# Kernel optimization log

Hardware: AMD Instinct MI355X
Metric: run time of the kernel (lower is better)

## Reference

```python
import jax, jax.numpy as jnp
import numpy as np

N, E, G = 50000, 1250000, 256
IN, H, OUT = 64, 64, 2


def _glorot(k, shape):
    fan = shape[0] + shape[1]
    return jax.random.normal(k, shape, jnp.float32) * np.float32(np.sqrt(2.0 / fan))


def setup_inputs() -> dict:
    key = jax.random.key(0)
    ks = jax.random.split(key, 24)
    inp = {
        "x": jax.random.normal(ks[0], (N, IN), jnp.float32),
        "edge_index": jax.random.randint(ks[1], (2, E), 0, N, dtype=jnp.int32),
        "edge_weight": jax.random.uniform(ks[2], (E,), jnp.float32),
        "batch": jnp.sort(jax.random.randint(ks[3], (N,), 0, G, dtype=jnp.int32)),
    }
    # TransformerConv layer 1 (in=IN -> out=H, heads=1, edge_dim=1)
    inp["Wq1"] = _glorot(ks[4], (IN, H)); inp["bq1"] = jnp.zeros((H,), jnp.float32)
    inp["Wk1"] = _glorot(ks[5], (IN, H)); inp["bk1"] = jnp.zeros((H,), jnp.float32)
    inp["Wv1"] = _glorot(ks[6], (IN, H)); inp["bv1"] = jnp.zeros((H,), jnp.float32)
    inp["We1"] = _glorot(ks[7], (1, H))
    inp["Ws1"] = _glorot(ks[8], (IN, H)); inp["bs1"] = jnp.zeros((H,), jnp.float32)
    # TransformerConv layer 2 (H -> H)
    inp["Wq2"] = _glorot(ks[9], (H, H)); inp["bq2"] = jnp.zeros((H,), jnp.float32)
    inp["Wk2"] = _glorot(ks[10], (H, H)); inp["bk2"] = jnp.zeros((H,), jnp.float32)
    inp["Wv2"] = _glorot(ks[11], (H, H)); inp["bv2"] = jnp.zeros((H,), jnp.float32)
    inp["We2"] = _glorot(ks[12], (1, H))
    inp["Ws2"] = _glorot(ks[13], (H, H)); inp["bs2"] = jnp.zeros((H,), jnp.float32)
    # final linear
    inp["Wl"] = _glorot(ks[14], (H, OUT)); inp["bl"] = jnp.zeros((OUT,), jnp.float32)
    return inp


def _tconv(x, src, dst, e_attr, Wq, bq, Wk, bk, Wv, bv, We, Ws, bs, n):
    # PyG TransformerConv, heads=1, concat=True, root_weight=True, beta=False.
    d = Wq.shape[1]
    q = (x @ Wq + bq)[dst]            # [E, d] gather at target nodes
    k = (x @ Wk + bk)[src]            # [E, d] gather at source nodes
    v = (x @ Wv + bv)[src]            # [E, d]
    e = e_attr @ We                   # [E, d] edge embedding (no bias in PyG)
    alpha = jnp.sum(q * (k + e), axis=-1) / jnp.sqrt(jnp.float32(d))  # [E]
    # segment softmax over incoming edges of each target node
    amax = jax.ops.segment_max(alpha, dst, num_segments=n)
    amax = jnp.where(jnp.isfinite(amax), amax, jnp.float32(0.0))
    ex = jnp.exp(alpha - amax[dst])
    denom = jax.ops.segment_sum(ex, dst, num_segments=n)
    w = ex / jnp.maximum(denom[dst], jnp.float32(1e-16))
    out = jax.ops.segment_sum(w[:, None] * (v + e), dst, num_segments=n)  # [n, d]
    return out + x @ Ws + bs          # skip connection (lin_skip)


def reference(x, edge_index, edge_weight, batch,
              Wq1, bq1, Wk1, bk1, Wv1, bv1, We1, Ws1, bs1,
              Wq2, bq2, Wk2, bk2, Wv2, bv2, We2, Ws2, bs2,
              Wl, bl):
    src, dst = edge_index[0], edge_index[1]
    ea = edge_weight[:, None]  # edge_weight.unsqueeze(-1), edge_dim=1
    n = x.shape[0]
    h = jax.nn.relu(_tconv(x, src, dst, ea, Wq1, bq1, Wk1, bk1, Wv1, bv1, We1, Ws1, bs1, n))
    h = jax.nn.relu(_tconv(h, src, dst, ea, Wq2, bq2, Wk2, bk2, Wv2, bv2, We2, Ws2, bs2, n))
    # global_mean_pool over batch ids
    cnt = jax.ops.segment_sum(jnp.ones((n,), jnp.float32), batch, num_segments=G)
    pooled = jax.ops.segment_sum(h, batch, num_segments=G) / jnp.maximum(cnt, 1.0)[:, None]
    return pooled @ Wl + bl
```

## Files before the change

kernel.cpp:

```cpp
#include <hip/hip_runtime.h>
#include <hip/hip_fp16.h>

#define NN 50000
#define NE 1250000
#define NE4 312500
#define NG 256
#define NBKT 782
#define BCAP 2048
#define TILE 4096
#define NTB 306
#define NLIN 999
#define FGRID 1332

#define QSCALE 0.18033688011112042f
#define EXP2 __builtin_amdgcn_exp2f

#if defined(__has_builtin)
#  if __has_builtin(__builtin_amdgcn_fdot2)
#    define HAS_FDOT2 1
#  endif
#endif

typedef _Float16 h2vec __attribute__((ext_vector_type(2)));

static __device__ __forceinline__ float fdot2f(unsigned a, unsigned b, float c) {
#ifdef HAS_FDOT2
    return __builtin_amdgcn_fdot2(__builtin_bit_cast(h2vec, a),
                                  __builtin_bit_cast(h2vec, b), c, false);
#else
    float2 fa = __half22float2(__builtin_bit_cast(__half2, a));
    float2 fb = __half22float2(__builtin_bit_cast(__half2, b));
    return fmaf(fa.x, fb.x, fmaf(fa.y, fb.y, c));
#endif
}

static __device__ __forceinline__ unsigned h2u(__half2 h) {
    return __builtin_bit_cast(unsigned, h);
}

static __device__ __forceinline__ void linear_body(
    const float* __restrict__ xin, int lid, int nblk,
    const float* __restrict__ Wq, const float* __restrict__ bq,
    const float* __restrict__ Wk, const float* __restrict__ bk,
    const float* __restrict__ Wv, const float* __restrict__ bv,
    const float* __restrict__ Ws, const float* __restrict__ bs,
    __half* __restrict__ qh, __half* __restrict__ kvh,
    float* __restrict__ agg, float* sx) {
    int tid = threadIdx.x;
    int mat = tid >> 6, feat = tid & 63;
    const float* W = mat == 0 ? Wq : mat == 1 ? Wk : mat == 2 ? Wv : Ws;
    const float* b = mat == 0 ? bq : mat == 1 ? bk : mat == 2 ? bv : bs;

    float wcol[64];
    #pragma unroll
    for (int k = 0; k < 64; k++) wcol[k] = W[k * 64 + feat];
    float bias = b[feat];
    int kvoff = feat + (mat == 2 ? 64 : 0);

    const float4* x4 = (const float4*)xin;

    for (int n0 = lid * 16; n0 < NN; n0 += nblk * 16) {
        __syncthreads();
        ((float4*)sx)[tid] = x4[n0 * 16 + tid];
        __syncthreads();
        for (int c = 0; c < 16; c++) {
            const float4* sxc = (const float4*)(sx + c * 64);
            float a0 = bias, a1 = 0.f, a2 = 0.f, a3 = 0.f;
            #pragma unroll
            for (int k4 = 0; k4 < 16; k4 += 4) {
                float4 v0 = sxc[k4 + 0], v1 = sxc[k4 + 1];
                float4 v2 = sxc[k4 + 2], v3 = sxc[k4 + 3];
                a0 = fmaf(v0.x, wcol[4 * k4 + 0], a0);
                a0 = fmaf(v0.y, wcol[4 * k4 + 1], a0);
                a0 = fmaf(v0.z, wcol[4 * k4 + 2], a0);
                a0 = fmaf(v0.w, wcol[4 * k4 + 3], a0);
                a1 = fmaf(v1.x, wcol[4 * k4 + 4], a1);
                a1 = fmaf(v1.y, wcol[4 * k4 + 5], a1);
                a1 = fmaf(v1.z, wcol[4 * k4 + 6], a1);
                a1 = fmaf(v1.w, wcol[4 * k4 + 7], a1);
                a2 = fmaf(v2.x, wcol[4 * k4 + 8], a2);
                a2 = fmaf(v2.y, wcol[4 * k4 + 9], a2);
                a2 = fmaf(v2.z, wcol[4 * k4 + 10], a2);
                a2 = fmaf(v2.w, wcol[4 * k4 + 11], a2);
                a3 = fmaf(v3.x, wcol[4 * k4 + 12], a3);
                a3 = fmaf(v3.y, wcol[4 * k4 + 13], a3);
                a3 = fmaf(v3.z, wcol[4 * k4 + 14], a3);
                a3 = fmaf(v3.w, wcol[4 * k4 + 15], a3);
            }
            float acc = (a0 + a1) + (a2 + a3);
            int nn = n0 + c;
            if (mat == 0)      qh[nn * 64 + feat] = __float2half(acc * QSCALE);
            else if (mat == 3) agg[nn * 64 + feat] = acc;
            else               kvh[nn * 128 + kvoff] = __float2half(acc);
        }
    }
}

static __device__ __forceinline__ void scatter_body(
    int bid, const int* __restrict__ src, const int* __restrict__ dst,
    const float* __restrict__ ew, int* __restrict__ gCursor,
    unsigned* __restrict__ bbuf, int* cnt) {
    int* base = cnt + NBKT;
    for (int i = threadIdx.x; i < NBKT; i += 256) cnt[i] = 0;
    __syncthreads();
    const int4* s4 = (const int4*)src;
    const int4* d4 = (const int4*)dst;
    const float4* w4 = (const float4*)ew;
    int b4 = bid * (TILE / 4);
    unsigned rec[16]; int bkt[16];
    #pragma unroll
    for (int j = 0; j < 4; j++) {
        int i4 = b4 + j * 256 + threadIdx.x;
        if (i4 < NE4) {
            int4 s = s4[i4]; int4 d = d4[i4]; float4 w = w4[i4];
            int b0 = d.x >> 6, b1 = d.y >> 6, b2 = d.z >> 6, b3 = d.w >> 6;
            bkt[4*j+0] = b0; bkt[4*j+1] = b1; bkt[4*j+2] = b2; bkt[4*j+3] = b3;
            rec[4*j+0] = (unsigned)s.x | ((unsigned)(d.x & 63) << 16) | ((unsigned)(w.x * 1023.f + 0.5f) << 22);
            rec[4*j+1] = (unsigned)s.y | ((unsigned)(d.y & 63) << 16) | ((unsigned)(w.y * 1023.f + 0.5f) << 22);
            rec[4*j+2] = (unsigned)s.z | ((unsigned)(d.z & 63) << 16) | ((unsigned)(w.z * 1023.f + 0.5f) << 22);
            rec[4*j+3] = (unsigned)s.w | ((unsigned)(d.w & 63) << 16) | ((unsigned)(w.w * 1023.f + 0.5f) << 22);
            atomicAdd(&cnt[b0], 1); atomicAdd(&cnt[b1], 1);
            atomicAdd(&cnt[b2], 1); atomicAdd(&cnt[b3], 1);
        } else {
            bkt[4*j+0] = -1; bkt[4*j+1] = -1; bkt[4*j+2] = -1; bkt[4*j+3] = -1;
        }
    }
    __syncthreads();
    for (int i = threadIdx.x; i < NBKT; i += 256)
        base[i] = cnt[i] ? (i << 11) + atomicAdd(&gCursor[i], cnt[i]) : 0;
    __syncthreads();
    #pragma unroll
    for (int j = 0; j < 16; j++) {
        if (bkt[j] >= 0) {
            int pos = atomicAdd(&base[bkt[j]], 1);
            if (pos < ((bkt[j] + 1) << 11)) bbuf[pos] = rec[j];
        }
    }
}

__global__ __launch_bounds__(256, 4)
void k_lin1_scat(const float* __restrict__ x,
                 const float* __restrict__ Wq, const float* __restrict__ bq,
                 const float* __restrict__ Wk, const float* __restrict__ bk,
                 const float* __restrict__ Wv, const float* __restrict__ bv,
                 const float* __restrict__ Ws, const float* __restrict__ bs,
                 __half* __restrict__ qh, __half* __restrict__ kvh,
                 float* __restrict__ agg,
                 const int* __restrict__ src, const int* __restrict__ dst,
                 const float* __restrict__ ew, int* __restrict__ gCursor,
                 unsigned* __restrict__ bbuf) {
    __shared__ __align__(16) char smem[2 * NBKT * 4];
    unsigned bx = blockIdx.x;
    if ((bx & 3) == 3) {
        int sid = bx >> 2;
        if (sid < NTB)
            scatter_body(sid, src, dst, ew, gCursor, bbuf, (int*)smem);
    } else {
        int lid = (int)bx - (int)(bx >> 2);
        linear_body(x, lid, NLIN, Wq, bq, Wk, bk, Wv, bv, Ws, bs,
                    qh, kvh, agg, (float*)smem);
    }
}

__global__ __launch_bounds__(256, 4)
void k_linear(const float* __restrict__ xin,
              const float* __restrict__ Wq, const float* __restrict__ bq,
              const float* __restrict__ Wk, const float* __restrict__ bk,
              const float* __restrict__ Wv, const float* __restrict__ bv,
              const float* __restrict__ Ws, const float* __restrict__ bs,
              __half* __restrict__ qh, __half* __restrict__ kvh,
              float* __restrict__ agg) {
    __shared__ __align__(16) float sx[16 * 64];
    linear_body(xin, blockIdx.x, 1024, Wq, bq, Wk, bk, Wv, bv, Ws, bs,
                qh, kvh, agg, sx);
}

__global__ void k_bsort(const int* __restrict__ gCursor, const unsigned* __restrict__ bbuf,
                        int* __restrict__ off, int* __restrict__ deg,
                        unsigned* __restrict__ pairP) {
    int b = blockIdx.x;
    int st = b << 11;
    int ce = gCursor[b]; if (ce > BCAP) ce = BCAP;
    __shared__ unsigned sbuf[BCAP];
    __shared__ int h[64];
    __shared__ int cur[64];
    if (threadIdx.x < 64) h[threadIdx.x] = 0;
    __syncthreads();
    for (int i = threadIdx.x; i < ce; i += 256) {
        unsigned r = bbuf[st + i];
        sbuf[i] = r;
        atomicAdd(&h[(r >> 16) & 63], 1);
    }
    __syncthreads();
    if (threadIdx.x < 64) {
        int v = h[threadIdx.x];
        int inc = v;
        #pragma unroll
        for (int o = 1; o < 64; o <<= 1) {
            int tmp = __shfl_up(inc, o);
            if (threadIdx.x >= o) inc += tmp;
        }
        int exc = st + inc - v;
        cur[threadIdx.x] = exc;
        int n = b * 64 + threadIdx.x;
        if (n < NN) { off[n] = exc; deg[n] = v; }
    }
    __syncthreads();
    for (int i = threadIdx.x; i < ce; i += 256) {
        unsigned r = sbuf[i];
        int pos = atomicAdd(&cur[(r >> 16) & 63], 1);
        float w = (float)(r >> 22) * (1.f / 1023.f);
        unsigned hw = (unsigned)__half_as_ushort(__float2half(w));
        pairP[pos] = (r & 0xFFFFu) | (hw << 16);
    }
}

__global__ void k_edge(const unsigned* __restrict__ pairP, const int* __restrict__ off,
                       const int* __restrict__ deg,
                       const __half* __restrict__ qh, const uint4* __restrict__ kv16,
                       const float* __restrict__ We, const float* __restrict__ aggin,
                       float* __restrict__ outp) {
    long gid = (long)blockIdx.x * 256 + threadIdx.x;
    int n = (int)(gid >> 6);
    if (n >= NN) return;
    int lane = threadIdx.x & 63;
    int g = lane >> 3, l = lane & 7;

    const uint4* q4 = (const uint4*)qh;
    uint4 qu = q4[n * 8 + l];
    const float4* wp = (const float4*)(We + l * 8);
    float4 wa = wp[0], wb = wp[1];
    unsigned we01 = h2u(__floats2half2_rn(wa.x, wa.y));
    unsigned we23 = h2u(__floats2half2_rn(wa.z, wa.w));
    unsigned we45 = h2u(__floats2half2_rn(wb.x, wb.y));
    unsigned we67 = h2u(__floats2half2_rn(wb.z, wb.w));

    int st = off[n], dg = deg[n];

    float qwe = fdot2f(qu.x, we01, fdot2f(qu.y, we23,
                fdot2f(qu.z, we45, fdot2f(qu.w, we67, 0.f))));
    qwe += __shfl_xor(qwe, 1); qwe += __shfl_xor(qwe, 2); qwe += __shfl_xor(qwe, 4);

    float den = 0.f, sw = 0.f;
    float acc[8] = {0.f, 0.f, 0.f, 0.f, 0.f, 0.f, 0.f, 0.f};

    auto edge = [&](unsigned pr, uint4 kk, uint4 vv) {
        float w = __half2float(__ushort_as_half((unsigned short)(pr >> 16)));
        float tA = fdot2f(qu.x, kk.x, fdot2f(qu.y, kk.y, 0.f));
        float tB = fdot2f(qu.z, kk.z, fdot2f(qu.w, kk.w, 0.f));
        float t = tA + tB;
        t += __shfl_xor(t, 1); t += __shfl_xor(t, 2); t += __shfl_xor(t, 4);
        t = fmaf(w, qwe, t);
        float p = EXP2(t);
        den += p;
        sw = fmaf(p, w, sw);
        float2 v0 = __half22float2(__builtin_bit_cast(__half2, vv.x));
        float2 v1 = __half22float2(__builtin_bit_cast(__half2, vv.y));
        float2 v2 = __half22float2(__builtin_bit_cast(__half2, vv.z));
        float2 v3 = __half22float2(__builtin_bit_cast(__half2, vv.w));
        acc[0] = fmaf(p, v0.x, acc[0]); acc[1] = fmaf(p, v0.y, acc[1]);
        acc[2] = fmaf(p, v1.x, acc[2]); acc[3] = fmaf(p, v1.y, acc[3]);
        acc[4] = fmaf(p, v2.x, acc[4]); acc[5] = fmaf(p, v2.y, acc[5]);
        acc[6] = fmaf(p, v3.x, acc[6]); acc[7] = fmaf(p, v3.y, acc[7]);
    };

    int nfull = dg >> 3;
    if (nfull > 0) {
        unsigned prA = pairP[st + g];
        unsigned prB = (nfull > 1) ? pairP[st + 8 + g] : 0u;
        unsigned rowA = prA & 0xFFFFu;
        uint4 kkA = kv16[rowA * 16 + l];
        uint4 vvA = kv16[rowA * 16 + 8 + l];
        for (int i = 0; i + 1 < nfull; i++) {
            unsigned prC = (i + 2 < nfull) ? pairP[st + (i + 2) * 8 + g] : 0u;
            unsigned rowB = prB & 0xFFFFu;
            uint4 kkB = kv16[rowB * 16 + l];
            uint4 vvB = kv16[rowB * 16 + 8 + l];
            edge(prA, kkA, vvA);
            prA = prB; kkA = kkB; vvA = vvB; prB = prC;
        }
        edge(prA, kkA, vvA);
    }
    int tl = nfull * 8 + g;
    if (tl < dg) {
        unsigned pr = pairP[st + tl];
        unsigned row = pr & 0xFFFFu;
        uint4 kk = kv16[row * 16 + l];
        uint4 vv = kv16[row * 16 + 8 + l];
        edge(pr, kk, vv);
    }

    #pragma unroll
    for (int o = 8; o <= 32; o <<= 1) {
        den += __shfl_xor(den, o);
        sw  += __shfl_xor(sw, o);
        #pragma unroll
        for (int j = 0; j < 8; j++) acc[j] += __shfl_xor(acc[j], o);
    }

    if (g == 0) {
        float inv = 1.f / fmaxf(den, 1e-16f);
        float swi = sw * inv;
        const float4* ain = (const float4*)(aggin + n * 64 + l * 8);
        float4 a0 = ain[0], a1 = ain[1];
        a0.x = fmaxf(fmaf(acc[0], inv, fmaf(swi, wa.x, a0.x)), 0.f);
        a0.y = fmaxf(fmaf(acc[1], inv, fmaf(swi, wa.y, a0.y)), 0.f);
        a0.z = fmaxf(fmaf(acc[2], inv, fmaf(swi, wa.z, a0.z)), 0.f);
        a0.w = fmaxf(fmaf(acc[3], inv, fmaf(swi, wa.w, a0.w)), 0.f);
        a1.x = fmaxf(fmaf(acc[4], inv, fmaf(swi, wb.x, a1.x)), 0.f);
        a1.y = fmaxf(fmaf(acc[5], inv, fmaf(swi, wb.y, a1.y)), 0.f);
        a1.z = fmaxf(fmaf(acc[6], inv, fmaf(swi, wb.z, a1.z)), 0.f);
        a1.w = fmaxf(fmaf(acc[7], inv, fmaf(swi, wb.w, a1.w)), 0.f);
        float4* ao = (float4*)(outp + n * 64 + l * 8);
        ao[0] = a0; ao[1] = a1;
    }
}

__global__ void k_final(const float* __restrict__ h, const int* __restrict__ batch,
                        const float* __restrict__ Wl, const float* __restrict__ bl,
                        float* __restrict__ out) {
    int g = blockIdx.x;
    int tid = threadIdx.x;
    int lo = 0, hi = NN;
    while (lo < hi) { int mid = (lo + hi) >> 1; if (batch[mid] < g) lo = mid + 1; else hi = mid; }
    int s0 = lo;
    hi = NN;
    while (lo < hi) { int mid = (lo + hi) >> 1; if (batch[mid] < g + 1) lo = mid + 1; else hi = mid; }
    int s1 = lo;

    int sub = tid >> 6, lane = tid & 63;
    float a = 0.f;
    for (int n = s0 + sub; n < s1; n += 4) a += h[n * 64 + lane];
    __shared__ float sred[4][64];
    sred[sub][lane] = a;
    __syncthreads();
    if (tid < 64) {
        float p = (sred[0][tid] + sred[1][tid] + sred[2][tid] + sred[3][tid])
                  / fmaxf((float)(s1 - s0), 1.f);
        float a0 = p * Wl[tid * 2 + 0];
        float a1 = p * Wl[tid * 2 + 1];
        #pragma unroll
        for (int o = 1; o < 64; o <<= 1) { a0 += __shfl_xor(a0, o); a1 += __shfl_xor(a1, o); }
        if (tid == 0) { out[g * 2 + 0] = a0 + bl[0]; out[g * 2 + 1] = a1 + bl[1]; }
    }
}

extern "C" void kernel_launch(void* const* d_in, const int* in_sizes, int n_in,
                              void* d_out, int out_size, void* d_ws, size_t ws_size,
                              hipStream_t stream) {
    const float* x    = (const float*)d_in[0];
    const int*   ei   = (const int*)d_in[1];
    const float* ew   = (const float*)d_in[2];
    const int*   batch= (const int*)d_in[3];
    const float *Wq1 = (const float*)d_in[4],  *bq1 = (const float*)d_in[5],
                *Wk1 = (const float*)d_in[6],  *bk1 = (const float*)d_in[7],
                *Wv1 = (const float*)d_in[8],  *bv1 = (const float*)d_in[9],
                *We1 = (const float*)d_in[10], *Ws1 = (const float*)d_in[11],
                *bs1 = (const float*)d_in[12],
                *Wq2 = (const float*)d_in[13], *bq2 = (const float*)d_in[14],
                *Wk2 = (const float*)d_in[15], *bk2 = (const float*)d_in[16],
                *Wv2 = (const float*)d_in[17], *bv2 = (const float*)d_in[18],
                *We2 = (const float*)d_in[19], *Ws2 = (const float*)d_in[20],
                *bs2 = (const float*)d_in[21],
                *Wl  = (const float*)d_in[22], *bl  = (const float*)d_in[23];
    const int* src = ei;
    const int* dst = ei + NE;
    float* out = (float*)d_out;

    float* p = (float*)d_ws;
    float* agg1 = p; p += (size_t)NN * 64;
    float* agg2 = p; p += (size_t)NN * 64;
    __half* qh  = (__half*)p; p += (size_t)NN * 32;
    __half* kvh = (__half*)p; p += (size_t)NN * 64;
    unsigned* bbuf  = (unsigned*)p; p += (size_t)NBKT * BCAP;
    unsigned* pairP = (unsigned*)p; p += (size_t)NBKT * BCAP;
    int* gCursor = (int*)p; p += NBKT;
    int* off     = (int*)p; p += NN;
    int* deg     = (int*)p; p += NN;

    dim3 b256(256);
    int wgrid = (int)(((long)NN * 64 + 255) / 256);

    hipMemsetAsync(gCursor, 0, NBKT * sizeof(int), stream);

    k_lin1_scat<<<FGRID, b256, 0, stream>>>(x, Wq1, bq1, Wk1, bk1, Wv1, bv1, Ws1, bs1,
                                            qh, kvh, agg1, src, dst, ew, gCursor, bbuf);
    k_bsort<<<NBKT, b256, 0, stream>>>(gCursor, bbuf, off, deg, pairP);

    k_edge<<<wgrid, b256, 0, stream>>>(pairP, off, deg, qh, (const uint4*)kvh, We1,
                                       agg1, agg1);

    k_linear<<<1024, b256, 0, stream>>>(agg1, Wq2, bq2, Wk2, bk2, Wv2, bv2, Ws2, bs2,
                                        qh, kvh, agg2);
    k_edge<<<wgrid, b256, 0, stream>>>(pairP, off, deg, qh, (const uint4*)kvh, We2,
                                       agg2, agg2);

    k_final<<<NG, b256, 0, stream>>>(agg2, batch, Wl, bl, out);
}
```

Measured before the change: 215.4 us.

## Split fused linear+scatter kernel into separate scatter and linear launches

Undoes the horizontal fusion of the first-layer projection with the edge bucket scatter. It now launches a standalone bucket-scatter kernel with a smaller tile (more blocks, fewer records per thread), then the bucket sort, then a separate layer-1 linear launch. This removes the role-dispatch branch, the shared-memory sizing compromise and the register pressure from the 16-record scatter path. In exchange it gives up overlap between the projection and the scatter and adds a kernel launch.

```diff
diff --git a/kernel.cpp b/kernel.cpp
--- a/kernel.cpp
+++ b/kernel.cpp
@@ -7,10 +7,8 @@
 #define NG 256
 #define NBKT 782
 #define BCAP 2048
-#define TILE 4096
-#define NTB 306
-#define NLIN 999
-#define FGRID 1332
+#define TILE 2048
+#define NTB 611
 
 #define QSCALE 0.18033688011112042f
 #define EXP2 __builtin_amdgcn_exp2f
@@ -38,14 +36,96 @@
     return __builtin_bit_cast(unsigned, h);
 }
 
-static __device__ __forceinline__ void linear_body(
-    const float* __restrict__ xin, int lid, int nblk,
-    const float* __restrict__ Wq, const float* __restrict__ bq,
-    const float* __restrict__ Wk, const float* __restrict__ bk,
-    const float* __restrict__ Wv, const float* __restrict__ bv,
-    const float* __restrict__ Ws, const float* __restrict__ bs,
-    __half* __restrict__ qh, __half* __restrict__ kvh,
-    float* __restrict__ agg, float* sx) {
+__global__ void k_bscatter(const int* __restrict__ src, const int* __restrict__ dst,
+                           const float* __restrict__ ew, int* __restrict__ gCursor,
+                           unsigned* __restrict__ bbuf) {
+    __shared__ int cnt[NBKT];
+    __shared__ int base[NBKT];
+    for (int i = threadIdx.x; i < NBKT; i += 256) cnt[i] = 0;
+    __syncthreads();
+    const int4* s4 = (const int4*)src;
+    const int4* d4 = (const int4*)dst;
+    const float4* w4 = (const float4*)ew;
+    int b4 = blockIdx.x * (TILE / 4);
+    unsigned rec[8]; int bkt[8];
+    #pragma unroll
+    for (int j = 0; j < 2; j++) {
+        int i4 = b4 + j * 256 + threadIdx.x;
+        if (i4 < NE4) {
+            int4 s = s4[i4]; int4 d = d4[i4]; float4 w = w4[i4];
+            int b0 = d.x >> 6, b1 = d.y >> 6, b2 = d.z >> 6, b3 = d.w >> 6;
+            bkt[4*j+0] = b0; bkt[4*j+1] = b1; bkt[4*j+2] = b2; bkt[4*j+3] = b3;
+            rec[4*j+0] = (unsigned)s.x | ((unsigned)(d.x & 63) << 16) | ((unsigned)(w.x * 1023.f + 0.5f) << 22);
+            rec[4*j+1] = (unsigned)s.y | ((unsigned)(d.y & 63) << 16) | ((unsigned)(w.y * 1023.f + 0.5f) << 22);
+            rec[4*j+2] = (unsigned)s.z | ((unsigned)(d.z & 63) << 16) | ((unsigned)(w.z * 1023.f + 0.5f) << 22);
+            rec[4*j+3] = (unsigned)s.w | ((unsigned)(d.w & 63) << 16) | ((unsigned)(w.w * 1023.f + 0.5f) << 22);
+            atomicAdd(&cnt[b0], 1); atomicAdd(&cnt[b1], 1);
+            atomicAdd(&cnt[b2], 1); atomicAdd(&cnt[b3], 1);
+        } else {
+            bkt[4*j+0] = -1; bkt[4*j+1] = -1; bkt[4*j+2] = -1; bkt[4*j+3] = -1;
+        }
+    }
+    __syncthreads();
+    for (int i = threadIdx.x; i < NBKT; i += 256)
+        base[i] = cnt[i] ? (i << 11) + atomicAdd(&gCursor[i], cnt[i]) : 0;
+    __syncthreads();
+    #pragma unroll
+    for (int j = 0; j < 8; j++) {
+        if (bkt[j] >= 0) {
+            int pos = atomicAdd(&base[bkt[j]], 1);
+            if (pos < ((bkt[j] + 1) << 11)) bbuf[pos] = rec[j];
+        }
+    }
+}
+
+__global__ void k_bsort(const int* __restrict__ gCursor, const unsigned* __restrict__ bbuf,
+                        int* __restrict__ off, int* __restrict__ deg,
+                        unsigned* __restrict__ pairP) {
+    int b = blockIdx.x;
+    int st = b << 11;
+    int ce = gCursor[b]; if (ce > BCAP) ce = BCAP;
+    __shared__ unsigned sbuf[BCAP];
+    __shared__ int h[64];
+    __shared__ int cur[64];
+    if (threadIdx.x < 64) h[threadIdx.x] = 0;
+    __syncthreads();
+    for (int i = threadIdx.x; i < ce; i += 256) {
+        unsigned r = bbuf[st + i];
+        sbuf[i] = r;
+        atomicAdd(&h[(r >> 16) & 63], 1);
+    }
+    __syncthreads();
+    if (threadIdx.x < 64) {
+        int v = h[threadIdx.x];
+        int inc = v;
+        #pragma unroll
+        for (int o = 1; o < 64; o <<= 1) {
+            int tmp = __shfl_up(inc, o);
+            if (threadIdx.x >= o) inc += tmp;
+        }
+        int exc = st + inc - v;
+        cur[threadIdx.x] = exc;
+        int n = b * 64 + threadIdx.x;
+        if (n < NN) { off[n] = exc; deg[n] = v; }
+    }
+    __syncthreads();
+    for (int i = threadIdx.x; i < ce; i += 256) {
+        unsigned r = sbuf[i];
+        int pos = atomicAdd(&cur[(r >> 16) & 63], 1);
+        float w = (float)(r >> 22) * (1.f / 1023.f);
+        unsigned hw = (unsigned)__half_as_ushort(__float2half(w));
+        pairP[pos] = (r & 0xFFFFu) | (hw << 16);
+    }
+}
+
+__global__ __launch_bounds__(256, 4)
+void k_linear(const float* __restrict__ xin,
+              const float* __restrict__ Wq, const float* __restrict__ bq,
+              const float* __restrict__ Wk, const float* __restrict__ bk,
+              const float* __restrict__ Wv, const float* __restrict__ bv,
+              const float* __restrict__ Ws, const float* __restrict__ bs,
+              __half* __restrict__ qh, __half* __restrict__ kvh,
+              float* __restrict__ agg) {
     int tid = threadIdx.x;
     int mat = tid >> 6, feat = tid & 63;
     const float* W = mat == 0 ? Wq : mat == 1 ? Wk : mat == 2 ? Wv : Ws;
@@ -57,9 +137,10 @@
     float bias = b[feat];
     int kvoff = feat + (mat == 2 ? 64 : 0);
 
+    __shared__ __align__(16) float sx[16 * 64];
     const float4* x4 = (const float4*)xin;
 
-    for (int n0 = lid * 16; n0 < NN; n0 += nblk * 16) {
+    for (int n0 = blockIdx.x * 16; n0 < NN; n0 += gridDim.x * 16) {
         __syncthreads();
         ((float4*)sx)[tid] = x4[n0 * 16 + tid];
         __syncthreads();
@@ -96,125 +177,6 @@
     }
 }
 
-static __device__ __forceinline__ void scatter_body(
-    int bid, const int* __restrict__ src, const int* __restrict__ dst,
-    const float* __restrict__ ew, int* __restrict__ gCursor,
-    unsigned* __restrict__ bbuf, int* cnt) {
-    int* base = cnt + NBKT;
-    for (int i = threadIdx.x; i < NBKT; i += 256) cnt[i] = 0;
-    __syncthreads();
-    const int4* s4 = (const int4*)src;
-    const int4* d4 = (const int4*)dst;
-    const float4* w4 = (const float4*)ew;
-    int b4 = bid * (TILE / 4);
-    unsigned rec[16]; int bkt[16];
-    #pragma unroll
-    for (int j = 0; j < 4; j++) {
-        int i4 = b4 + j * 256 + threadIdx.x;
-        if (i4 < NE4) {
-            int4 s = s4[i4]; int4 d = d4[i4]; float4 w = w4[i4];
-            int b0 = d.x >> 6, b1 = d.y >> 6, b2 = d.z >> 6, b3 = d.w >> 6;
-            bkt[4*j+0] = b0; bkt[4*j+1] = b1; bkt[4*j+2] = b2; bkt[4*j+3] = b3;
-            rec[4*j+0] = (unsigned)s.x | ((unsigned)(d.x & 63) << 16) | ((unsigned)(w.x * 1023.f + 0.5f) << 22);
-            rec[4*j+1] = (unsigned)s.y | ((unsigned)(d.y & 63) << 16) | ((unsigned)(w.y * 1023.f + 0.5f) << 22);
-            rec[4*j+2] = (unsigned)s.z | ((unsigned)(d.z & 63) << 16) | ((unsigned)(w.z * 1023.f + 0.5f) << 22);
-            rec[4*j+3] = (unsigned)s.w | ((unsigned)(d.w & 63) << 16) | ((unsigned)(w.w * 1023.f + 0.5f) << 22);
-            atomicAdd(&cnt[b0], 1); atomicAdd(&cnt[b1], 1);
-            atomicAdd(&cnt[b2], 1); atomicAdd(&cnt[b3], 1);
-        } else {
-            bkt[4*j+0] = -1; bkt[4*j+1] = -1; bkt[4*j+2] = -1; bkt[4*j+3] = -1;
-        }
-    }
-    __syncthreads();
-    for (int i = threadIdx.x; i < NBKT; i += 256)
-        base[i] = cnt[i] ? (i << 11) + atomicAdd(&gCursor[i], cnt[i]) : 0;
-    __syncthreads();
-    #pragma unroll
-    for (int j = 0; j < 16; j++) {
-        if (bkt[j] >= 0) {
-            int pos = atomicAdd(&base[bkt[j]], 1);
-            if (pos < ((bkt[j] + 1) << 11)) bbuf[pos] = rec[j];
-        }
-    }
-}
-
-__global__ __launch_bounds__(256, 4)
-void k_lin1_scat(const float* __restrict__ x,
-                 const float* __restrict__ Wq, const float* __restrict__ bq,
-                 const float* __restrict__ Wk, const float* __restrict__ bk,
-                 const float* __restrict__ Wv, const float* __restrict__ bv,
-                 const float* __restrict__ Ws, const float* __restrict__ bs,
-                 __half* __restrict__ qh, __half* __restrict__ kvh,
-                 float* __restrict__ agg,
-                 const int* __restrict__ src, const int* __restrict__ dst,
-                 const float* __restrict__ ew, int* __restrict__ gCursor,
-                 unsigned* __restrict__ bbuf) {
-    __shared__ __align__(16) char smem[2 * NBKT * 4];
-    unsigned bx = blockIdx.x;
-    if ((bx & 3) == 3) {
-        int sid = bx >> 2;
-        if (sid < NTB)
-            scatter_body(sid, src, dst, ew, gCursor, bbuf, (int*)smem);
-    } else {
-        int lid = (int)bx - (int)(bx >> 2);
-        linear_body(x, lid, NLIN, Wq, bq, Wk, bk, Wv, bv, Ws, bs,
-                    qh, kvh, agg, (float*)smem);
-    }
-}
-
-__global__ __launch_bounds__(256, 4)
-void k_linear(const float* __restrict__ xin,
-              const float* __restrict__ Wq, const float* __restrict__ bq,
-              const float* __restrict__ Wk, const float* __restrict__ bk,
-              const float* __restrict__ Wv, const float* __restrict__ bv,
-              const float* __restrict__ Ws, const float* __restrict__ bs,
-              __half* __restrict__ qh, __half* __restrict__ kvh,
-              float* __restrict__ agg) {
-    __shared__ __align__(16) float sx[16 * 64];
-    linear_body(xin, blockIdx.x, 1024, Wq, bq, Wk, bk, Wv, bv, Ws, bs,
-                qh, kvh, agg, sx);
-}
-
-__global__ void k_bsort(const int* __restrict__ gCursor, const unsigned* __restrict__ bbuf,
-                        int* __restrict__ off, int* __restrict__ deg,
-                        unsigned* __restrict__ pairP) {
-    int b = blockIdx.x;
-    int st = b << 11;
-    int ce = gCursor[b]; if (ce > BCAP) ce = BCAP;
-    __shared__ unsigned sbuf[BCAP];
-    __shared__ int h[64];
-    __shared__ int cur[64];
-    if (threadIdx.x < 64) h[threadIdx.x] = 0;
-    __syncthreads();
-    for (int i = threadIdx.x; i < ce; i += 256) {
-        unsigned r = bbuf[st + i];
-        sbuf[i] = r;
-        atomicAdd(&h[(r >> 16) & 63], 1);
-    }
-    __syncthreads();
-    if (threadIdx.x < 64) {
-        int v = h[threadIdx.x];
-        int inc = v;
-        #pragma unroll
-        for (int o = 1; o < 64; o <<= 1) {
-            int tmp = __shfl_up(inc, o);
-            if (threadIdx.x >= o) inc += tmp;
-        }
-        int exc = st + inc - v;
-        cur[threadIdx.x] = exc;
-        int n = b * 64 + threadIdx.x;
-        if (n < NN) { off[n] = exc; deg[n] = v; }
-    }
-    __syncthreads();
-    for (int i = threadIdx.x; i < ce; i += 256) {
-        unsigned r = sbuf[i];
-        int pos = atomicAdd(&cur[(r >> 16) & 63], 1);
-        float w = (float)(r >> 22) * (1.f / 1023.f);
-        unsigned hw = (unsigned)__half_as_ushort(__float2half(w));
-        pairP[pos] = (r & 0xFFFFu) | (hw << 16);
-    }
-}
-
 __global__ void k_edge(const unsigned* __restrict__ pairP, const int* __restrict__ off,
                        const int* __restrict__ deg,
                        const __half* __restrict__ qh, const uint4* __restrict__ kv16,
@@ -383,10 +345,11 @@
 
     hipMemsetAsync(gCursor, 0, NBKT * sizeof(int), stream);
 
-    k_lin1_scat<<<FGRID, b256, 0, stream>>>(x, Wq1, bq1, Wk1, bk1, Wv1, bv1, Ws1, bs1,
-                                            qh, kvh, agg1, src, dst, ew, gCursor, bbuf);
+    k_bscatter<<<NTB, b256, 0, stream>>>(src, dst, ew, gCursor, bbuf);
     k_bsort<<<NBKT, b256, 0, stream>>>(gCursor, bbuf, off, deg, pairP);
 
+    k_linear<<<1024, b256, 0, stream>>>(x, Wq1, bq1, Wk1, bk1, Wv1, bv1, Ws1, bs1,
+                                        qh, kvh, agg1);
     k_edge<<<wgrid, b256, 0, stream>>>(pairP, off, deg, qh, (const uint4*)kvh, We1,
                                        agg1, agg1);
 
```

Measured after the change: 224.6 us. +4.3%, slower.
